# Kernel optimization log

Measured on AMD Instinct MI355X. Metric: run time of the kernel, lower is better.

Reference implementation:

```python
import jax, jax.numpy as jnp
import numpy as np
import math

B = 16; L = 1024; CIN = 3; COUT = 1; D = 128; K = 16; DEPTH = 4
EPS = 1e-5; GRID_RANGE = 1.0


def _haar_basis(L):
    # Orthonormal Haar wavelet basis, rows of V (L, L). L must be power of 2.
    V = np.zeros((L, L), dtype=np.float64)
    V[0, :] = 1.0 / math.sqrt(L)
    r, s = 1, 1
    while s < L and r < L:
        block = 2 * s
        amp = 1.0 / math.sqrt(block)
        for j in range(L // block):
            st = j * block
            V[r, st:st + s] = amp
            V[r, st + s:st + block] = -amp
            r += 1
            if r >= L:
                break
        s *= 2
    return V


def _phi_f(L, k):
    # rFFT of top-k Haar basis rows, complex64 (matches build_stu_basis_rfft)
    V = _haar_basis(L)
    return jnp.asarray(np.fft.rfft(V, axis=-1)[:k].astype(np.complex64))


def setup_inputs() -> dict:
    key = jax.random.key(0)
    ks = jax.random.split(key, 8)

    def rn(k, shape, scale):
        return jax.random.normal(k, shape, dtype=jnp.float32) * scale

    return {
        "x": jax.random.normal(ks[0], (B, CIN, L), dtype=jnp.float32),
        "lift_w": rn(ks[1], (D, CIN + 1), 1.0 / math.sqrt(CIN + 1)),  # conv1x1 weight
        "lift_b": jnp.zeros((D,), jnp.float32),
        "Phi_f": _phi_f(L, K),                                        # (K, L//2+1) complex64 buffer
        "theta": rn(ks[2], (DEPTH, K, D, D), 1.0 / math.sqrt(D)),
        "ln_g": jnp.ones((DEPTH, D), jnp.float32),
        "ln_b": jnp.zeros((DEPTH, D), jnp.float32),
        "fc1_w": rn(ks[3], (DEPTH, 2 * D, D), 1.0 / math.sqrt(D)),
        "fc1_b": jnp.zeros((DEPTH, 2 * D), jnp.float32),
        "fc2_w": rn(ks[4], (DEPTH, D, 2 * D), 1.0 / math.sqrt(2 * D)),
        "fc2_b": jnp.zeros((DEPTH, D), jnp.float32),
        "head_w": rn(ks[5], (COUT, D), 1.0 / math.sqrt(D)),
        "head_b": jnp.zeros((COUT,), jnp.float32),
    }


def _forward(x, lift_w, lift_b, Phi_f, theta, ln_g, ln_b,
             fc1_w, fc1_b, fc2_w, fc2_b, head_w, head_b):
    # add_grid: append linspace coord channel -> (B, CIN+1, L)
    coords = jnp.linspace(0.0, GRID_RANGE, L, dtype=x.dtype)
    coords = jnp.broadcast_to(coords, (x.shape[0], 1, L))
    xg = jnp.concatenate([x, coords], axis=1)

    # LocalLift1D with kernel_size=1 == pointwise linear over channels
    h = jnp.einsum('bcl,dc->bdl', xg, lift_w) + lift_b[None, :, None]

    Phic = jnp.conj(Phi_f)  # (K, Lr)
    for i in range(DEPTH):
        # LayerNorm over channel dim (torch LN on transposed (B,L,D))
        mu = jnp.mean(h, axis=1, keepdims=True)
        var = jnp.var(h, axis=1, keepdims=True)
        z = (h - mu) / jnp.sqrt(var + EPS) * ln_g[i][None, :, None] + ln_b[i][None, :, None]

        Xf = jnp.fft.rfft(z, axis=-1)                       # (B, D, Lr)
        Uf = Xf[:, :, None, :] * Phic[None, None, :, :]     # (B, D, K, Lr)
        U = jnp.fft.irfft(Uf, n=L, axis=-1)                 # (B, D, K, L)

        # fused einsum('bdln,lhd->bhln') + sum over l(=k)
        S = jnp.einsum('bdkn,khd->bhn', U, theta[i])        # (B, D, L)

        # pointwise MLP (conv1x1 -> GELU -> conv1x1), residual
        H1 = jax.nn.gelu(jnp.einsum('bdl,hd->bhl', S, fc1_w[i]) + fc1_b[i][None, :, None],
                         approximate=False)
        h = h + jnp.einsum('bhl,dh->bdl', H1, fc2_w[i]) + fc2_b[i][None, :, None]

    # head: conv1x1 lifting_dim -> out_dim
    return jnp.einsum('bdl,od->bol', h, head_w) + head_b[None, :, None]


def reference(x, lift_w, lift_b, Phi_f, theta, ln_g, ln_b,
              fc1_w, fc1_b, fc2_w, fc2_b, head_w, head_b):
    return _forward(x, lift_w, lift_b, Phi_f, theta, ln_g, ln_b,
                    fc1_w, fc1_b, fc2_w, fc2_b, head_w, head_b)
```

## Files before the change

### kernel.cpp

```cpp
#include <hip/hip_runtime.h>
#include <math.h>

#define BB 16
#define LL 1024
#define DD 128
#define BL (BB*LL)
#define NDEPTH 4
#define EPSF 1e-5f

typedef unsigned short u16;
typedef short bf16x8 __attribute__((ext_vector_type(8)));
typedef short bf16x4 __attribute__((ext_vector_type(4)));
typedef float f32x4 __attribute__((ext_vector_type(4)));

static __device__ __forceinline__ u16 f2bf(float x) {
    unsigned u = __float_as_uint(x);
    u = u + 0x7fffu + ((u >> 16) & 1u);
    return (u16)(u >> 16);
}
static __device__ __forceinline__ float bf2f(short v) {
    return __uint_as_float(((unsigned)(unsigned short)v) << 16);
}

#define DZ_B  0
#define S_B   15360
#define H1_B  23552
#define ZS_B  39936
#define C_B   40448
#define RST_B 40960
#define MRS_B 41088
#define LDS_TOT 41216

#define N_TH (4*15*16384)
#define N_W1 (4*32768)
#define N_W2 (4*32768)
#define N_TH0 (4*16384)
__global__ __launch_bounds__(256) void cvt_kernel(const float* __restrict__ theta,
        const float* __restrict__ fc1w, const float* __restrict__ fc2w,
        u16* __restrict__ thf, u16* __restrict__ w1f, u16* __restrict__ w2f,
        u16* __restrict__ th0f) {
    int o = blockIdx.x * 256 + threadIdx.x;
    if (o < N_TH) {
        int j = o & 7, ln = (o >> 3) & 63, c = (o >> 9) & 3, f = (o >> 11) & 7;
        int slab = o >> 14;
        int layer = slab / 15, kk = slab - layer * 15;
        int h = f * 16 + (ln & 15), d = 32 * c + 8 * (ln >> 4) + j;
        thf[o] = f2bf(theta[(((size_t)layer * 16 + kk + 1) * 128 + h) * 128 + d]);
    } else if (o < N_TH + N_W1) {
        int o2 = o - N_TH;
        int j = o2 & 7, ln = (o2 >> 3) & 63, c = (o2 >> 9) & 3, f = (o2 >> 11) & 15;
        int layer = o2 >> 15;
        int m = f * 16 + (ln & 15), d = 32 * c + 8 * (ln >> 4) + j;
        w1f[o2] = f2bf(fc1w[(size_t)layer * 32768 + m * 128 + d]);
    } else if (o < N_TH + N_W1 + N_W2) {
        int o2 = o - (N_TH + N_W1);
        int j = o2 & 7, ln = (o2 >> 3) & 63, c = (o2 >> 9) & 7, f = (o2 >> 12) & 7;
        int layer = o2 >> 15;
        int d = f * 16 + (ln & 15), m = 32 * c + 8 * (ln >> 4) + j;
        w2f[o2] = f2bf(fc2w[(size_t)layer * 32768 + d * 256 + m]);
    } else if (o < N_TH + N_W1 + N_W2 + N_TH0) {
        int o2 = o - (N_TH + N_W1 + N_W2);
        int layer = o2 >> 14, idx = o2 & 16383;
        th0f[o2] = f2bf(theta[(size_t)layer * 262144 + idx]);
    }
}

__global__ __launch_bounds__(512) void prep0_kernel(const float* __restrict__ x,
        const float* __restrict__ lw, const float* __restrict__ lb,
        float* __restrict__ H, float2* __restrict__ stats,
        float* __restrict__ P1p, float* __restrict__ P2p) {
    __shared__ char lds[16384 + 256];
    float* rst = (float*)(lds + 16384);
    float* mrs = (float*)(lds + 16384 + 128);
    int b = blockIdx.y, nblk = blockIdx.x, t0 = nblk * 32, tid = threadIdx.x;

    #pragma unroll
    for (int it = 0; it < 2; ++it) {
        int idx = it * 512 + tid;
        int r = idx >> 5, d0 = (idx & 31) * 4;
        int l = t0 + r;
        float x0 = x[(size_t)b * 3072 + l];
        float x1 = x[(size_t)b * 3072 + 1024 + l];
        float x2 = x[(size_t)b * 3072 + 2048 + l];
        float coord = (float)l * (1.0f / 1023.0f);
        f32x4 hv;
        #pragma unroll
        for (int q = 0; q < 4; ++q) {
            int d = d0 + q;
            float4 w = *(const float4*)(lw + d * 4);
            hv[q] = lb[d] + w.x * x0 + w.y * x1 + w.z * x2 + w.w * coord;
        }
        *(f32x4*)(H + ((size_t)b * 1024 + l) * 128 + d0) = hv;
        int byte = r * 512 + ((d0 * 4) ^ ((r & 7) << 4));
        *(f32x4*)(lds + byte) = hv;
    }
    __syncthreads();
    {
        int t = tid >> 4, q = tid & 15;
        float s = 0.f, sq = 0.f;
        #pragma unroll
        for (int dd = 0; dd < 8; dd += 4) {
            int d = q * 8 + dd;
            int byte = t * 512 + ((d * 4) ^ ((t & 7) << 4));
            f32x4 v = *(const f32x4*)(lds + byte);
            s += v[0] + v[1] + v[2] + v[3];
            sq += v[0]*v[0] + v[1]*v[1] + v[2]*v[2] + v[3]*v[3];
        }
        #pragma unroll
        for (int o = 1; o < 16; o <<= 1) {
            s += __shfl_xor(s, o, 64); sq += __shfl_xor(sq, o, 64);
        }
        if (q == 0) {
            float mu = s * (1.f / 128.f);
            float var = sq * (1.f / 128.f) - mu * mu;
            float rs = rsqrtf(var + EPSF);
            stats[(size_t)b * 1024 + t0 + t] = make_float2(mu, rs);
            rst[t] = rs; mrs[t] = mu * rs;
        }
    }
    __syncthreads();
    if (tid < 128) {
        float s = 0.f;
        #pragma unroll 8
        for (int t = 0; t < 32; ++t) {
            int byte = t * 512 + ((tid * 4) ^ ((t & 7) << 4));
            s += *(const float*)(lds + byte) * rst[t];
        }
        P1p[((size_t)b * 32 + nblk) * 128 + tid] = s;
    } else if (tid == 128) {
        float s = 0.f;
        for (int t = 0; t < 32; ++t) s += mrs[t];
        P2p[b * 32 + nblk] = s;
    }
}

template<int LAST>
__global__ __launch_bounds__(512, 4) void mega_kernel(
        const float* __restrict__ Hin, const float2* __restrict__ stin,
        const float* __restrict__ lng, const float* __restrict__ lnb,
        const u16* __restrict__ thf, const u16* __restrict__ th0f,
        const u16* __restrict__ w1f, const float* __restrict__ b1,
        const u16* __restrict__ w2f, const float* __restrict__ b2,
        float* __restrict__ Hout, float2* __restrict__ stout,
        const float* __restrict__ P1in, const float* __restrict__ P2in,
        float* __restrict__ P1out, float* __restrict__ P2out,
        const float* __restrict__ hwp, const float* __restrict__ hbp,
        float* __restrict__ out) {
    __shared__ char lds[LDS_TOT];
    int b = blockIdx.y, nblk = blockIdx.x, n0 = nblk * 32, tid = threadIdx.x;
    const float inv_s2 = 0.70710678118654752f;

    const float* Hb = Hin + (size_t)b * 1024 * 128;
    const float2* stb = stin + (size_t)b * 1024;
    for (int c = tid; c < 60 * 16; c += 512) {
        int r = c >> 4, d0 = (c & 15) * 8;
        int gr = (n0 + r) & 1023, g1 = (n0 + r + 1) & 1023;
        const float* ha = Hb + (size_t)gr * 128 + d0;
        const float* hc = Hb + (size_t)g1 * 128 + d0;
        float2 sa = stb[gr], sb = stb[g1];
        u16 tmp[8];
        #pragma unroll
        for (int j = 0; j < 8; ++j) {
            float za = (ha[j] - sa.x) * sa.y;
            float zc = (hc[j] - sb.x) * sb.y;
            tmp[j] = f2bf((za - zc) * inv_s2 * lng[d0 + j]);
        }
        int byte = r * 256 + ((d0 * 2) ^ ((r & 7) << 4));
        *(bf16x8*)(lds + byte) = *(bf16x8*)tmp;
    }
    if (tid < 128) {
        float s = 0.f;
        #pragma unroll 8
        for (int j = 0; j < 32; ++j) s += P1in[((size_t)b * 32 + j) * 128 + tid];
        float p2 = 0.f;
        #pragma unroll 8
        for (int j = 0; j < 32; ++j) p2 += P2in[b * 32 + j];
        ((float*)(lds + ZS_B))[tid] = lng[tid] * (s - p2) + 1024.0f * lnb[tid];
    }
    __syncthreads();

    int wave = tid >> 6, lane = tid & 63;
    int lm = lane & 15, lk = (lane >> 4) * 8;
    f32x4 zero4 = {0.f, 0.f, 0.f, 0.f};

    {
        int h = tid >> 2, q = tid & 3;
        const u16* th0 = th0f + h * 128 + q * 32;
        const float* zs = (const float*)(lds + ZS_B) + q * 32;
        float acc = 0.f;
        #pragma unroll
        for (int c = 0; c < 4; ++c) {
            bf16x8 tv = *(const bf16x8*)(th0 + c * 8);
            #pragma unroll
            for (int j = 0; j < 8; ++j) acc += bf2f(tv[j]) * zs[c * 8 + j];
        }
        acc += __shfl_xor(acc, 1, 64);
        acc += __shfl_xor(acc, 2, 64);
        if (q == 0) ((float*)(lds + C_B))[h] = acc * (1.0f / 32.0f);
    }
    __syncthreads();

    f32x4 accS[2] = {zero4, zero4};
    {
        const u16* thl = thf + (size_t)lane * 8 + (size_t)wave * 2048;
        bf16x8 bufA[4], bufB[4];
        #pragma unroll
        for (int c4 = 0; c4 < 4; ++c4)
            bufA[c4] = *(const bf16x8*)(thl + c4 * 512);
        #pragma unroll
        for (int kp = 0; kp < 7; ++kp) {
            int kk = kp * 2;
            #pragma unroll
            for (int c4 = 0; c4 < 4; ++c4)
                bufB[c4] = *(const bf16x8*)(thl + (size_t)(kk + 1) * 16384 + c4 * 512);
            #pragma unroll
            for (int c4 = 0; c4 < 4; ++c4) {
                #pragma unroll
                for (int nt = 0; nt < 2; ++nt) {
                    int trow = nt * 16 + lm + 2 * kk;
                    int byte = trow * 256 + (((c4 * 32 + lk) * 2) ^ ((trow & 7) << 4));
                    bf16x8 bfr = *(const bf16x8*)(lds + byte);
                    accS[nt] = __builtin_amdgcn_mfma_f32_16x16x32_bf16(bufA[c4], bfr, accS[nt], 0, 0, 0);
                }
            }
            #pragma unroll
            for (int c4 = 0; c4 < 4; ++c4)
                bufA[c4] = *(const bf16x8*)(thl + (size_t)(kk + 2) * 16384 + c4 * 512);
            #pragma unroll
            for (int c4 = 0; c4 < 4; ++c4) {
                #pragma unroll
                for (int nt = 0; nt < 2; ++nt) {
                    int trow = nt * 16 + lm + 2 * (kk + 1);
                    int byte = trow * 256 + (((c4 * 32 + lk) * 2) ^ ((trow & 7) << 4));
                    bf16x8 bfr = *(const bf16x8*)(lds + byte);
                    accS[nt] = __builtin_amdgcn_mfma_f32_16x16x32_bf16(bufB[c4], bfr, accS[nt], 0, 0, 0);
                }
            }
        }
        #pragma unroll
        for (int c4 = 0; c4 < 4; ++c4) {
            #pragma unroll
            for (int nt = 0; nt < 2; ++nt) {
                int trow = nt * 16 + lm + 28;
                int byte = trow * 256 + (((c4 * 32 + lk) * 2) ^ ((trow & 7) << 4));
                bf16x8 bfr = *(const bf16x8*)(lds + byte);
                accS[nt] = __builtin_amdgcn_mfma_f32_16x16x32_bf16(bufA[c4], bfr, accS[nt], 0, 0, 0);
            }
        }
    }

    {
        int h0 = wave * 16 + (lane >> 4) * 4;
        f32x4 cv = *(const f32x4*)(lds + C_B + h0 * 4);
        #pragma unroll
        for (int nt = 0; nt < 2; ++nt) {
            int tl = nt * 16 + lm;
            u16 o[4];
            #pragma unroll
            for (int r = 0; r < 4; ++r) o[r] = f2bf(accS[nt][r] + cv[r]);
            int byte = S_B + tl * 256 + ((h0 * 2) ^ ((tl & 7) << 4));
            *(bf16x4*)(lds + byte) = *(bf16x4*)o;
        }
    }
    __syncthreads();

    {
        f32x4 acc1[2][2];
        #pragma unroll
        for (int mt = 0; mt < 2; ++mt)
            #pragma unroll
            for (int nt = 0; nt < 2; ++nt) acc1[mt][nt] = zero4;
        const u16* w1l = w1f + (size_t)lane * 8;
        #pragma unroll
        for (int c4 = 0; c4 < 4; ++c4) {
            bf16x8 afr[2], bfr[2];
            #pragma unroll
            for (int mt = 0; mt < 2; ++mt)
                afr[mt] = *(const bf16x8*)(w1l + ((size_t)((wave * 2 + mt) * 4 + c4) << 9));
            #pragma unroll
            for (int nt = 0; nt < 2; ++nt) {
                int tl = nt * 16 + lm;
                int byte = S_B + tl * 256 + (((c4 * 32 + lk) * 2) ^ ((tl & 7) << 4));
                bfr[nt] = *(const bf16x8*)(lds + byte);
            }
            #pragma unroll
            for (int mt = 0; mt < 2; ++mt)
                #pragma unroll
                for (int nt = 0; nt < 2; ++nt)
                    acc1[mt][nt] = __builtin_amdgcn_mfma_f32_16x16x32_bf16(
                        afr[mt], bfr[nt], acc1[mt][nt], 0, 0, 0);
        }
        #pragma unroll
        for (int mt = 0; mt < 2; ++mt) {
            int mo = wave * 32 + mt * 16 + (lane >> 4) * 4;
            f32x4 bb4 = *(const f32x4*)(b1 + mo);
            #pragma unroll
            for (int nt = 0; nt < 2; ++nt) {
                int tl = nt * 16 + lm;
                u16 o[4];
                #pragma unroll
                for (int r = 0; r < 4; ++r) {
                    float xv = acc1[mt][nt][r] + bb4[r];
                    o[r] = f2bf(0.5f * xv * (1.0f + erff(xv * 0.70710678118654752f)));
                }
                int byte = H1_B + tl * 512 + ((mo * 2) ^ ((tl & 7) << 4));
                *(bf16x4*)(lds + byte) = *(bf16x4*)o;
            }
        }
    }
    __syncthreads();

    f32x4 acc2[2] = {zero4, zero4};
    {
        const u16* w2l = w2f + (size_t)lane * 8;
        #pragma unroll
        for (int c8 = 0; c8 < 8; ++c8) {
            bf16x8 afr = *(const bf16x8*)(w2l + ((size_t)(wave * 8 + c8) << 9));
            #pragma unroll
            for (int nt = 0; nt < 2; ++nt) {
                int tl = nt * 16 + lm;
                int byte = H1_B + tl * 512 + (((c8 * 32 + lk) * 2) ^ ((tl & 7) << 4));
                bf16x8 bfr = *(const bf16x8*)(lds + byte);
                acc2[nt] = __builtin_amdgcn_mfma_f32_16x16x32_bf16(afr, bfr, acc2[nt], 0, 0, 0);
            }
        }
    }
    __syncthreads();

    {
        int dbase = wave * 16 + (lane >> 4) * 4;
        #pragma unroll
        for (int nt = 0; nt < 2; ++nt) {
            int tl = nt * 16 + lm;
            int byte = H1_B + tl * 512 + ((dbase * 4) ^ ((tl & 7) << 4));
            *(f32x4*)(lds + byte) = acc2[nt];
        }
    }
    __syncthreads();

    {
        const float* Hrow = Hin + ((size_t)b * 1024 + n0) * 128;
        float* Horow = Hout + ((size_t)b * 1024 + n0) * 128;
        #pragma unroll
        for (int it = 0; it < 2; ++it) {
            int idx = it * 512 + tid;
            int r = idx >> 5, d0 = (idx & 31) * 4;
            int byte = H1_B + r * 512 + ((d0 * 4) ^ ((r & 7) << 4));
            f32x4 v = *(const f32x4*)(lds + byte);
            f32x4 bb = *(const f32x4*)(b2 + d0);
            f32x4 hv = *(const f32x4*)(Hrow + (size_t)r * 128 + d0);
            hv = hv + v + bb;
            if (LAST) {
                f32x4 wv = *(const f32x4*)(hwp + d0);
                float s = hv[0]*wv[0] + hv[1]*wv[1] + hv[2]*wv[2] + hv[3]*wv[3];
                #pragma unroll
                for (int o = 1; o < 32; o <<= 1) s += __shfl_xor(s, o, 64);
                if ((lane & 31) == 0) out[(size_t)b * 1024 + n0 + r] = s + hbp[0];
            } else {
                *(f32x4*)(Horow + (size_t)r * 128 + d0) = hv;
                *(f32x4*)(lds + byte) = hv;
            }
        }
    }
    if (!LAST) {
        __syncthreads();
        float* rst = (float*)(lds + RST_B);
        float* mrs = (float*)(lds + MRS_B);
        {
            int t = tid >> 4, q = tid & 15;
            float s = 0.f, sq = 0.f;
            #pragma unroll
            for (int dd = 0; dd < 8; dd += 4) {
                int d = q * 8 + dd;
                int byte = H1_B + t * 512 + ((d * 4) ^ ((t & 7) << 4));
                f32x4 v = *(const f32x4*)(lds + byte);
                s += v[0] + v[1] + v[2] + v[3];
                sq += v[0]*v[0] + v[1]*v[1] + v[2]*v[2] + v[3]*v[3];
            }
            #pragma unroll
            for (int o = 1; o < 16; o <<= 1) {
                s += __shfl_xor(s, o, 64); sq += __shfl_xor(sq, o, 64);
            }
            if (q == 0) {
                float mu = s * (1.f / 128.f);
                float var = sq * (1.f / 128.f) - mu * mu;
                float rs = rsqrtf(var + EPSF);
                stout[(size_t)b * 1024 + n0 + t] = make_float2(mu, rs);
                rst[t] = rs; mrs[t] = mu * rs;
            }
        }
        __syncthreads();
        if (tid < 128) {
            float s = 0.f;
            #pragma unroll 8
            for (int t = 0; t < 32; ++t) {
                int byte = H1_B + t * 512 + ((tid * 4) ^ ((t & 7) << 4));
                s += *(const float*)(lds + byte) * rst[t];
            }
            P1out[((size_t)b * 32 + nblk) * 128 + tid] = s;
        } else if (tid == 128) {
            float s = 0.f;
            for (int t = 0; t < 32; ++t) s += mrs[t];
            P2out[b * 32 + nblk] = s;
        }
    }
}

extern "C" void kernel_launch(void* const* d_in, const int* in_sizes, int n_in,
                              void* d_out, int out_size, void* d_ws, size_t ws_size,
                              hipStream_t stream) {
    const float* x     = (const float*)d_in[0];
    const float* lw    = (const float*)d_in[1];
    const float* lb    = (const float*)d_in[2];
    const float* theta = (const float*)d_in[4];
    const float* ln_g  = (const float*)d_in[5];
    const float* ln_b  = (const float*)d_in[6];
    const float* fc1w  = (const float*)d_in[7];
    const float* fc1b  = (const float*)d_in[8];
    const float* fc2w  = (const float*)d_in[9];
    const float* fc2b  = (const float*)d_in[10];
    const float* hw    = (const float*)d_in[11];
    const float* hb    = (const float*)d_in[12];

    float* ws = (float*)d_ws;
    float* H_A = ws;
    float* H_B = H_A + (size_t)BL * DD;
    float2* st_A = (float2*)(H_B + (size_t)BL * DD);
    float2* st_B = st_A + BL;
    float* P1A = (float*)(st_B + BL);
    float* P1B = P1A + 16 * 32 * 128;
    float* P2A = P1B + 16 * 32 * 128;
    float* P2B = P2A + 512;
    u16* thf  = (u16*)(P2B + 512);
    u16* w1f  = thf + N_TH;
    u16* w2f  = w1f + N_W1;
    u16* th0f = w2f + N_W2;

    cvt_kernel<<<(N_TH + N_W1 + N_W2 + N_TH0) / 256, 256, 0, stream>>>(
        theta, fc1w, fc2w, thf, w1f, w2f, th0f);
    prep0_kernel<<<dim3(32, 16), 512, 0, stream>>>(x, lw, lb, H_A, st_A, P1A, P2A);

    float* Hi = H_A; float* Ho = H_B;
    float2* sti = st_A; float2* sto = st_B;
    float* p1i = P1A; float* p1o = P1B;
    float* p2i = P2A; float* p2o = P2B;
    for (int i = 0; i < NDEPTH; ++i) {
        if (i < NDEPTH - 1) {
            mega_kernel<0><<<dim3(32, 16), 512, 0, stream>>>(
                Hi, sti, ln_g + i * 128, ln_b + i * 128,
                thf + (size_t)i * 15 * 16384, th0f + (size_t)i * 16384,
                w1f + (size_t)i * 32768, fc1b + i * 256,
                w2f + (size_t)i * 32768, fc2b + i * 128,
                Ho, sto, p1i, p2i, p1o, p2o, hw, hb, (float*)d_out);
        } else {
            mega_kernel<1><<<dim3(32, 16), 512, 0, stream>>>(
                Hi, sti, ln_g + i * 128, ln_b + i * 128,
                thf + (size_t)i * 15 * 16384, th0f + (size_t)i * 16384,
                w1f + (size_t)i * 32768, fc1b + i * 256,
                w2f + (size_t)i * 32768, fc2b + i * 128,
                Ho, sto, p1i, p2i, p1o, p2o, hw, hb, (float*)d_out);
        }
        float* t;
        t = Hi; Hi = Ho; Ho = t;
        float2* ts = sti; sti = sto; sto = ts;
        t = p1i; p1i = p1o; p1o = t;
        t = p2i; p2i = p2o; p2o = t;
    }
}
```

Baseline: 148.2 us.

## Double sequence tile per block and split spectral GEMM across k-halves

Each block now processes 64 sequence positions instead of 32, halving the grid to 256 blocks. The spectral theta GEMM is restructured so each wave computes a 64x32 output tile, with the 15 k-slices split between two wave groups and the partial sums reduced through LDS. The MLP GEMMs are widened to four N tiles so each weight fragment loaded from global memory is reused across twice as many positions. In exchange, LDS use grows, the occupancy hint drops to two blocks per CU, and fewer blocks may underfill the 256 CUs.

```diff
diff --git a/kernel.cpp b/kernel.cpp
--- a/kernel.cpp
+++ b/kernel.cpp
@@ -22,14 +22,13 @@
     return __uint_as_float(((unsigned)(unsigned short)v) << 16);
 }
 
-#define DZ_B  0
-#define S_B   15360
-#define H1_B  23552
-#define ZS_B  39936
-#define C_B   40448
-#define RST_B 40960
-#define MRS_B 41088
-#define LDS_TOT 41216
+#define R0_B  0
+#define S_B   32768
+#define ZS_B  49152
+#define C_B   49664
+#define RST_B 50176
+#define MRS_B 50432
+#define LDS_TOT 50688
 
 #define N_TH (4*15*16384)
 #define N_W1 (4*32768)
@@ -69,13 +68,13 @@
         const float* __restrict__ lw, const float* __restrict__ lb,
         float* __restrict__ H, float2* __restrict__ stats,
         float* __restrict__ P1p, float* __restrict__ P2p) {
-    __shared__ char lds[16384 + 256];
-    float* rst = (float*)(lds + 16384);
-    float* mrs = (float*)(lds + 16384 + 128);
-    int b = blockIdx.y, nblk = blockIdx.x, t0 = nblk * 32, tid = threadIdx.x;
+    __shared__ char lds[33280];
+    float* rst = (float*)(lds + 32768);
+    float* mrs = (float*)(lds + 32768 + 256);
+    int b = blockIdx.y, nblk = blockIdx.x, t0 = nblk * 64, tid = threadIdx.x;
 
     #pragma unroll
-    for (int it = 0; it < 2; ++it) {
+    for (int it = 0; it < 4; ++it) {
         int idx = it * 512 + tid;
         int r = idx >> 5, d0 = (idx & 31) * 4;
         int l = t0 + r;
@@ -96,18 +95,18 @@
     }
     __syncthreads();
     {
-        int t = tid >> 4, q = tid & 15;
+        int t = tid >> 3, q = tid & 7;
         float s = 0.f, sq = 0.f;
         #pragma unroll
-        for (int dd = 0; dd < 8; dd += 4) {
-            int d = q * 8 + dd;
+        for (int dd = 0; dd < 16; dd += 4) {
+            int d = q * 16 + dd;
             int byte = t * 512 + ((d * 4) ^ ((t & 7) << 4));
             f32x4 v = *(const f32x4*)(lds + byte);
             s += v[0] + v[1] + v[2] + v[3];
             sq += v[0]*v[0] + v[1]*v[1] + v[2]*v[2] + v[3]*v[3];
         }
         #pragma unroll
-        for (int o = 1; o < 16; o <<= 1) {
+        for (int o = 1; o < 8; o <<= 1) {
             s += __shfl_xor(s, o, 64); sq += __shfl_xor(sq, o, 64);
         }
         if (q == 0) {
@@ -122,20 +121,20 @@
     if (tid < 128) {
         float s = 0.f;
         #pragma unroll 8
-        for (int t = 0; t < 32; ++t) {
+        for (int t = 0; t < 64; ++t) {
             int byte = t * 512 + ((tid * 4) ^ ((t & 7) << 4));
             s += *(const float*)(lds + byte) * rst[t];
         }
-        P1p[((size_t)b * 32 + nblk) * 128 + tid] = s;
+        P1p[((size_t)b * 16 + nblk) * 128 + tid] = s;
     } else if (tid == 128) {
         float s = 0.f;
-        for (int t = 0; t < 32; ++t) s += mrs[t];
-        P2p[b * 32 + nblk] = s;
+        for (int t = 0; t < 64; ++t) s += mrs[t];
+        P2p[b * 16 + nblk] = s;
     }
 }
 
 template<int LAST>
-__global__ __launch_bounds__(512, 4) void mega_kernel(
+__global__ __launch_bounds__(512, 2) void mega_kernel(
         const float* __restrict__ Hin, const float2* __restrict__ stin,
         const float* __restrict__ lng, const float* __restrict__ lnb,
         const u16* __restrict__ thf, const u16* __restrict__ th0f,
@@ -147,12 +146,12 @@
         const float* __restrict__ hwp, const float* __restrict__ hbp,
         float* __restrict__ out) {
     __shared__ char lds[LDS_TOT];
-    int b = blockIdx.y, nblk = blockIdx.x, n0 = nblk * 32, tid = threadIdx.x;
+    int b = blockIdx.y, nblk = blockIdx.x, n0 = nblk * 64, tid = threadIdx.x;
     const float inv_s2 = 0.70710678118654752f;
 
     const float* Hb = Hin + (size_t)b * 1024 * 128;
     const float2* stb = stin + (size_t)b * 1024;
-    for (int c = tid; c < 60 * 16; c += 512) {
+    for (int c = tid; c < 92 * 16; c += 512) {
         int r = c >> 4, d0 = (c & 15) * 8;
         int gr = (n0 + r) & 1023, g1 = (n0 + r + 1) & 1023;
         const float* ha = Hb + (size_t)gr * 128 + d0;
@@ -170,11 +169,11 @@
     }
     if (tid < 128) {
         float s = 0.f;
-        #pragma unroll 8
-        for (int j = 0; j < 32; ++j) s += P1in[((size_t)b * 32 + j) * 128 + tid];
+        #pragma unroll
+        for (int j = 0; j < 16; ++j) s += P1in[((size_t)b * 16 + j) * 128 + tid];
         float p2 = 0.f;
-        #pragma unroll 8
-        for (int j = 0; j < 32; ++j) p2 += P2in[b * 32 + j];
+        #pragma unroll
+        for (int j = 0; j < 16; ++j) p2 += P2in[b * 16 + j];
         ((float*)(lds + ZS_B))[tid] = lng[tid] * (s - p2) + 1024.0f * lnb[tid];
     }
     __syncthreads();
@@ -200,85 +199,83 @@
     }
     __syncthreads();
 
-    f32x4 accS[2] = {zero4, zero4};
-    {
-        const u16* thl = thf + (size_t)lane * 8 + (size_t)wave * 2048;
-        bf16x8 bufA[4], bufB[4];
-        #pragma unroll
-        for (int c4 = 0; c4 < 4; ++c4)
-            bufA[c4] = *(const bf16x8*)(thl + c4 * 512);
-        #pragma unroll
-        for (int kp = 0; kp < 7; ++kp) {
-            int kk = kp * 2;
-            #pragma unroll
-            for (int c4 = 0; c4 < 4; ++c4)
-                bufB[c4] = *(const bf16x8*)(thl + (size_t)(kk + 1) * 16384 + c4 * 512);
+    int ks = wave >> 2, hg = (wave >> 1) & 1, tg = wave & 1;
+    f32x4 acc[4][2];
+    #pragma unroll
+    for (int mt = 0; mt < 4; ++mt)
+        #pragma unroll
+        for (int nt = 0; nt < 2; ++nt) acc[mt][nt] = zero4;
+    {
+        const u16* thl = thf + (size_t)lane * 8;
+        int kk0 = ks ? 8 : 0, kk1 = ks ? 15 : 8;
+        for (int kk = kk0; kk < kk1; ++kk) {
             #pragma unroll
             for (int c4 = 0; c4 < 4; ++c4) {
+                bf16x8 afr[4], bfr[2];
+                #pragma unroll
+                for (int mt = 0; mt < 4; ++mt)
+                    afr[mt] = *(const bf16x8*)(thl + ((size_t)((kk * 8 + hg * 4 + mt) * 4 + c4) << 9));
                 #pragma unroll
                 for (int nt = 0; nt < 2; ++nt) {
-                    int trow = nt * 16 + lm + 2 * kk;
+                    int trow = tg * 32 + nt * 16 + lm + 2 * kk;
                     int byte = trow * 256 + (((c4 * 32 + lk) * 2) ^ ((trow & 7) << 4));
-                    bf16x8 bfr = *(const bf16x8*)(lds + byte);
-                    accS[nt] = __builtin_amdgcn_mfma_f32_16x16x32_bf16(bufA[c4], bfr, accS[nt], 0, 0, 0);
+                    bfr[nt] = *(const bf16x8*)(lds + byte);
                 }
-            }
-            #pragma unroll
-            for (int c4 = 0; c4 < 4; ++c4)
-                bufA[c4] = *(const bf16x8*)(thl + (size_t)(kk + 2) * 16384 + c4 * 512);
-            #pragma unroll
-            for (int c4 = 0; c4 < 4; ++c4) {
-                #pragma unroll
-                for (int nt = 0; nt < 2; ++nt) {
-                    int trow = nt * 16 + lm + 2 * (kk + 1);
-                    int byte = trow * 256 + (((c4 * 32 + lk) * 2) ^ ((trow & 7) << 4));
-                    bf16x8 bfr = *(const bf16x8*)(lds + byte);
-                    accS[nt] = __builtin_amdgcn_mfma_f32_16x16x32_bf16(bufB[c4], bfr, accS[nt], 0, 0, 0);
-                }
-            }
-        }
+                #pragma unroll
+                for (int mt = 0; mt < 4; ++mt)
+                    #pragma unroll
+                    for (int nt = 0; nt < 2; ++nt)
+                        acc[mt][nt] = __builtin_amdgcn_mfma_f32_16x16x32_bf16(
+                            afr[mt], bfr[nt], acc[mt][nt], 0, 0, 0);
+            }
+        }
+    }
+    __syncthreads();
+    if (ks == 1) {
+        int slot = hg * 2 + tg;
+        #pragma unroll
+        for (int mt = 0; mt < 4; ++mt)
+            #pragma unroll
+            for (int nt = 0; nt < 2; ++nt)
+                *(f32x4*)(lds + R0_B + slot * 8192 + (mt * 2 + nt) * 1024 + lane * 16) = acc[mt][nt];
+    }
+    __syncthreads();
+    if (ks == 0) {
+        int slot = hg * 2 + tg;
+        const float* Cl = (const float*)(lds + C_B);
+        #pragma unroll
+        for (int mt = 0; mt < 4; ++mt) {
+            int h0 = hg * 64 + mt * 16 + (lane >> 4) * 4;
+            f32x4 cv = *(const f32x4*)(Cl + h0);
+            #pragma unroll
+            for (int nt = 0; nt < 2; ++nt) {
+                f32x4 p = *(const f32x4*)(lds + R0_B + slot * 8192 + (mt * 2 + nt) * 1024 + lane * 16);
+                int tl = tg * 32 + nt * 16 + lm;
+                u16 o[4];
+                #pragma unroll
+                for (int r = 0; r < 4; ++r) o[r] = f2bf(acc[mt][nt][r] + p[r] + cv[r]);
+                int byte = S_B + tl * 256 + ((h0 * 2) ^ ((tl & 7) << 4));
+                *(bf16x4*)(lds + byte) = *(bf16x4*)o;
+            }
+        }
+    }
+    __syncthreads();
+
+    {
+        f32x4 acc1[2][4];
+        #pragma unroll
+        for (int mt = 0; mt < 2; ++mt)
+            #pragma unroll
+            for (int nt = 0; nt < 4; ++nt) acc1[mt][nt] = zero4;
+        const u16* w1l = w1f + (size_t)lane * 8;
         #pragma unroll
         for (int c4 = 0; c4 < 4; ++c4) {
-            #pragma unroll
-            for (int nt = 0; nt < 2; ++nt) {
-                int trow = nt * 16 + lm + 28;
-                int byte = trow * 256 + (((c4 * 32 + lk) * 2) ^ ((trow & 7) << 4));
-                bf16x8 bfr = *(const bf16x8*)(lds + byte);
-                accS[nt] = __builtin_amdgcn_mfma_f32_16x16x32_bf16(bufA[c4], bfr, accS[nt], 0, 0, 0);
-            }
-        }
-    }
-
-    {
-        int h0 = wave * 16 + (lane >> 4) * 4;
-        f32x4 cv = *(const f32x4*)(lds + C_B + h0 * 4);
-        #pragma unroll
-        for (int nt = 0; nt < 2; ++nt) {
-            int tl = nt * 16 + lm;
-            u16 o[4];
-            #pragma unroll
-            for (int r = 0; r < 4; ++r) o[r] = f2bf(accS[nt][r] + cv[r]);
-            int byte = S_B + tl * 256 + ((h0 * 2) ^ ((tl & 7) << 4));
-            *(bf16x4*)(lds + byte) = *(bf16x4*)o;
-        }
-    }
-    __syncthreads();
-
-    {
-        f32x4 acc1[2][2];
-        #pragma unroll
-        for (int mt = 0; mt < 2; ++mt)
-            #pragma unroll
-            for (int nt = 0; nt < 2; ++nt) acc1[mt][nt] = zero4;
-        const u16* w1l = w1f + (size_t)lane * 8;
-        #pragma unroll
-        for (int c4 = 0; c4 < 4; ++c4) {
-            bf16x8 afr[2], bfr[2];
+            bf16x8 afr[2], bfr[4];
             #pragma unroll
             for (int mt = 0; mt < 2; ++mt)
                 afr[mt] = *(const bf16x8*)(w1l + ((size_t)((wave * 2 + mt) * 4 + c4) << 9));
             #pragma unroll
-            for (int nt = 0; nt < 2; ++nt) {
+            for (int nt = 0; nt < 4; ++nt) {
                 int tl = nt * 16 + lm;
                 int byte = S_B + tl * 256 + (((c4 * 32 + lk) * 2) ^ ((tl & 7) << 4));
                 bfr[nt] = *(const bf16x8*)(lds + byte);
@@ -286,7 +283,7 @@
             #pragma unroll
             for (int mt = 0; mt < 2; ++mt)
                 #pragma unroll
-                for (int nt = 0; nt < 2; ++nt)
+                for (int nt = 0; nt < 4; ++nt)
                     acc1[mt][nt] = __builtin_amdgcn_mfma_f32_16x16x32_bf16(
                         afr[mt], bfr[nt], acc1[mt][nt], 0, 0, 0);
         }
@@ -295,7 +292,7 @@
             int mo = wave * 32 + mt * 16 + (lane >> 4) * 4;
             f32x4 bb4 = *(const f32x4*)(b1 + mo);
             #pragma unroll
-            for (int nt = 0; nt < 2; ++nt) {
+            for (int nt = 0; nt < 4; ++nt) {
                 int tl = nt * 16 + lm;
                 u16 o[4];
                 #pragma unroll
@@ -303,23 +300,25 @@
                     float xv = acc1[mt][nt][r] + bb4[r];
                     o[r] = f2bf(0.5f * xv * (1.0f + erff(xv * 0.70710678118654752f)));
                 }
-                int byte = H1_B + tl * 512 + ((mo * 2) ^ ((tl & 7) << 4));
+                int byte = R0_B + tl * 512 + ((mo * 2) ^ ((tl & 7) << 4));
                 *(bf16x4*)(lds + byte) = *(bf16x4*)o;
             }
         }
     }
     __syncthreads();
 
-    f32x4 acc2[2] = {zero4, zero4};
+    f32x4 acc2[4];
+    #pragma unroll
+    for (int nt = 0; nt < 4; ++nt) acc2[nt] = zero4;
     {
         const u16* w2l = w2f + (size_t)lane * 8;
         #pragma unroll
         for (int c8 = 0; c8 < 8; ++c8) {
             bf16x8 afr = *(const bf16x8*)(w2l + ((size_t)(wave * 8 + c8) << 9));
             #pragma unroll
-            for (int nt = 0; nt < 2; ++nt) {
+            for (int nt = 0; nt < 4; ++nt) {
                 int tl = nt * 16 + lm;
-                int byte = H1_B + tl * 512 + (((c8 * 32 + lk) * 2) ^ ((tl & 7) << 4));
+                int byte = R0_B + tl * 512 + (((c8 * 32 + lk) * 2) ^ ((tl & 7) << 4));
                 bf16x8 bfr = *(const bf16x8*)(lds + byte);
                 acc2[nt] = __builtin_amdgcn_mfma_f32_16x16x32_bf16(afr, bfr, acc2[nt], 0, 0, 0);
             }
@@ -330,9 +329,9 @@
     {
         int dbase = wave * 16 + (lane >> 4) * 4;
         #pragma unroll
-        for (int nt = 0; nt < 2; ++nt) {
+        for (int nt = 0; nt < 4; ++nt) {
             int tl = nt * 16 + lm;
-            int byte = H1_B + tl * 512 + ((dbase * 4) ^ ((tl & 7) << 4));
+            int byte = R0_B + tl * 512 + ((dbase * 4) ^ ((tl & 7) << 4));
             *(f32x4*)(lds + byte) = acc2[nt];
         }
     }
@@ -342,10 +341,10 @@
         const float* Hrow = Hin + ((size_t)b * 1024 + n0) * 128;
         float* Horow = Hout + ((size_t)b * 1024 + n0) * 128;
         #pragma unroll
-        for (int it = 0; it < 2; ++it) {
+        for (int it = 0; it < 4; ++it) {
             int idx = it * 512 + tid;
             int r = idx >> 5, d0 = (idx & 31) * 4;
-            int byte = H1_B + r * 512 + ((d0 * 4) ^ ((r & 7) << 4));
+            int byte = R0_B + r * 512 + ((d0 * 4) ^ ((r & 7) << 4));
             f32x4 v = *(const f32x4*)(lds + byte);
             f32x4 bb = *(const f32x4*)(b2 + d0);
             f32x4 hv = *(const f32x4*)(Hrow + (size_t)r * 128 + d0);
@@ -367,18 +366,18 @@
         float* rst = (float*)(lds + RST_B);
         float* mrs = (float*)(lds + MRS_B);
         {
-            int t = tid >> 4, q = tid & 15;
+            int t = tid >> 3, q = tid & 7;
             float s = 0.f, sq = 0.f;
             #pragma unroll
-            for (int dd = 0; dd < 8; dd += 4) {
-                int d = q * 8 + dd;
-                int byte = H1_B + t * 512 + ((d * 4) ^ ((t & 7) << 4));
+            for (int dd = 0; dd < 16; dd += 4) {
+                int d = q * 16 + dd;
+                int byte = R0_B + t * 512 + ((d * 4) ^ ((t & 7) << 4));
                 f32x4 v = *(const f32x4*)(lds + byte);
                 s += v[0] + v[1] + v[2] + v[3];
                 sq += v[0]*v[0] + v[1]*v[1] + v[2]*v[2] + v[3]*v[3];
             }
             #pragma unroll
-            for (int o = 1; o < 16; o <<= 1) {
+            for (int o = 1; o < 8; o <<= 1) {
                 s += __shfl_xor(s, o, 64); sq += __shfl_xor(sq, o, 64);
             }
             if (q == 0) {
@@ -393,15 +392,15 @@
         if (tid < 128) {
             float s = 0.f;
             #pragma unroll 8
-            for (int t = 0; t < 32; ++t) {
-                int byte = H1_B + t * 512 + ((tid * 4) ^ ((t & 7) << 4));
+            for (int t = 0; t < 64; ++t) {
+                int byte = R0_B + t * 512 + ((tid * 4) ^ ((t & 7) << 4));
                 s += *(const float*)(lds + byte) * rst[t];
             }
-            P1out[((size_t)b * 32 + nblk) * 128 + tid] = s;
+            P1out[((size_t)b * 16 + nblk) * 128 + tid] = s;
         } else if (tid == 128) {
             float s = 0.f;
-            for (int t = 0; t < 32; ++t) s += mrs[t];
-            P2out[b * 32 + nblk] = s;
+            for (int t = 0; t < 64; ++t) s += mrs[t];
+            P2out[b * 16 + nblk] = s;
         }
     }
 }
@@ -428,17 +427,17 @@
     float2* st_A = (float2*)(H_B + (size_t)BL * DD);
     float2* st_B = st_A + BL;
     float* P1A = (float*)(st_B + BL);
-    float* P1B = P1A + 16 * 32 * 128;
-    float* P2A = P1B + 16 * 32 * 128;
-    float* P2B = P2A + 512;
-    u16* thf  = (u16*)(P2B + 512);
+    float* P1B = P1A + 16 * 16 * 128;
+    float* P2A = P1B + 16 * 16 * 128;
+    float* P2B = P2A + 256;
+    u16* thf  = (u16*)(P2B + 256);
     u16* w1f  = thf + N_TH;
     u16* w2f  = w1f + N_W1;
     u16* th0f = w2f + N_W2;
 
     cvt_kernel<<<(N_TH + N_W1 + N_W2 + N_TH0) / 256, 256, 0, stream>>>(
         theta, fc1w, fc2w, thf, w1f, w2f, th0f);
-    prep0_kernel<<<dim3(32, 16), 512, 0, stream>>>(x, lw, lb, H_A, st_A, P1A, P2A);
+    prep0_kernel<<<dim3(16, 16), 512, 0, stream>>>(x, lw, lb, H_A, st_A, P1A, P2A);
 
     float* Hi = H_A; float* Ho = H_B;
     float2* sti = st_A; float2* sto = st_B;
@@ -446,14 +445,14 @@
     float* p2i = P2A; float* p2o = P2B;
     for (int i = 0; i < NDEPTH; ++i) {
         if (i < NDEPTH - 1) {
-            mega_kernel<0><<<dim3(32, 16), 512, 0, stream>>>(
+            mega_kernel<0><<<dim3(16, 16), 512, 0, stream>>>(
                 Hi, sti, ln_g + i * 128, ln_b + i * 128,
                 thf + (size_t)i * 15 * 16384, th0f + (size_t)i * 16384,
                 w1f + (size_t)i * 32768, fc1b + i * 256,
                 w2f + (size_t)i * 32768, fc2b + i * 128,
                 Ho, sto, p1i, p2i, p1o, p2o, hw, hb, (float*)d_out);
         } else {
-            mega_kernel<1><<<dim3(32, 16), 512, 0, stream>>>(
+            mega_kernel<1><<<dim3(16, 16), 512, 0, stream>>>(
                 Hi, sti, ln_g + i * 128, ln_b + i * 128,
                 thf + (size_t)i * 15 * 16384, th0f + (size_t)i * 16384,
                 w1f + (size_t)i * 32768, fc1b + i * 256,
```

New measurement: 160.9 us. 8.6% more time.
